# Kernel optimization log

Hardware: AMD Instinct MI355X
Metric: run time of the kernel (lower is better)

The kernel has to match this reference:

```python
import jax, jax.numpy as jnp
import numpy as np

B, T, N = 16, 1024, 512        # batch, time tokens, neurons
DK_T, DK_S = 64, 128           # key dims (temporal, spatial)
# dim_T = N, dim_S = T, dim_value_T = N (required by cross einsum), heads = 1


def setup_inputs() -> dict:
    key = jax.random.key(0)
    ks = jax.random.split(key, 11)
    return {
        "x_T": jax.random.normal(ks[0], (B, T, N), jnp.float32),
        "x_S": jax.random.normal(ks[1], (B, N, T), jnp.float32),
        "Wq_T": jax.random.normal(ks[2], (N, DK_T), jnp.float32) * 0.05,
        "Wk_T": jax.random.normal(ks[3], (N, DK_T), jnp.float32) * 0.05,
        "Wv_T": jax.random.normal(ks[4], (N, N), jnp.float32) * 0.05,
        "Wq_S": jax.random.normal(ks[5], (T, DK_S), jnp.float32) * 0.05,
        "Wk_S": jax.random.normal(ks[6], (T, DK_S), jnp.float32) * 0.05,
        "Wout_T": jax.random.normal(ks[7], (N, N), jnp.float32) * 0.05,
        "bout_T": jax.random.normal(ks[8], (N,), jnp.float32) * 0.05,
        "bias_T": jax.random.normal(ks[9], (1, 1, 1, DK_T), jnp.float32),
        "bias_S": jax.random.normal(ks[10], (1, 1, 1, DK_S), jnp.float32),
    }


def reference(x_T, x_S, Wq_T, Wk_T, Wv_T, Wq_S, Wk_S, Wout_T, bout_T, bias_T, bias_S):
    scale_T = DK_T ** -0.5
    scale_S = DK_S ** -0.5
    # Temporal attention: tokens along time axis, heads=1 -> add h axis
    q_T = (x_T @ Wq_T)[:, None] * scale_T          # [b,1,t,dk_T]
    k_T = (x_T @ Wk_T)[:, None]                    # [b,1,t,dk_T]
    v_T = (x_T @ Wv_T)[:, None]                    # [b,1,t,n]  (dim_value_T = n)
    logits_T = jnp.einsum('bhid,bhjd->bhij', q_T + bias_T, k_T)  # [b,1,t,t]
    attn_T = jax.nn.softmax(logits_T, axis=-1)
    out_T = jnp.einsum('bhij,bhjd->bhid', attn_T, v_T)            # [b,1,t,n]
    # Spatial attention: tokens along neuron axis
    q_S = (x_S @ Wq_S)[:, None] * scale_S          # [b,1,n,dk_S]
    k_S = (x_S @ Wk_S)[:, None]                    # [b,1,n,dk_S]
    logits_S = jnp.einsum('bhid,bhjd->bhij', q_S + bias_S, k_S)   # [b,1,n,n]
    attn_S = jax.nn.softmax(logits_S, axis=-1)
    # spatial_temporal_1 cross combination: attn_S mixes the neuron axis of out_T
    out_T = jnp.einsum('bhij,bhtj->bhti', attn_S, out_T)          # [b,1,t,n]
    out_T = out_T.reshape(B, T, N)                 # 'b h t d -> b t (h d)'
    out_T = out_T @ Wout_T + bout_T                # to_out_T
    return jnp.transpose(out_T, (0, 2, 1))         # [b, n, t]
```

## Files before the change

### kernel.cpp

```cpp
#include <hip/hip_runtime.h>
#include <cstddef>

typedef short short8 __attribute__((ext_vector_type(8)));
typedef unsigned short ushortx8 __attribute__((ext_vector_type(8)));
typedef unsigned short ushortx4 __attribute__((ext_vector_type(4)));
typedef float floatx4 __attribute__((ext_vector_type(4)));

__device__ __forceinline__ unsigned int bf16_rne(float x) {
    unsigned int u = __float_as_uint(x);
    return (u + 0x7fffu + ((u >> 16) & 1u)) >> 16;
}

__device__ __forceinline__ void split4(const floatx4 v,
                                       unsigned long long& hp,
                                       unsigned long long& lp) {
    unsigned int h[4], l[4];
    #pragma unroll
    for (int j = 0; j < 4; ++j) {
        h[j] = bf16_rne(v[j]);
        float hf = __uint_as_float(h[j] << 16);
        l[j] = bf16_rne(v[j] - hf);
    }
    hp = (unsigned long long)(h[0] | (h[1] << 16)) |
         ((unsigned long long)(h[2] | (h[3] << 16)) << 32);
    lp = (unsigned long long)(l[0] | (l[1] << 16)) |
         ((unsigned long long)(l[2] | (l[3] << 16)) << 32);
}

__device__ __forceinline__ unsigned long long pack_hi4(const floatx4 v) {
    unsigned int h0 = bf16_rne(v[0]), h1 = bf16_rne(v[1]);
    unsigned int h2 = bf16_rne(v[2]), h3 = bf16_rne(v[3]);
    return (unsigned long long)(h0 | (h1 << 16)) |
           ((unsigned long long)(h2 | (h3 << 16)) << 32);
}

__global__ __launch_bounds__(256)
void convert_split(const float* __restrict__ in, long n,
                   unsigned short* __restrict__ H, unsigned short* __restrict__ L)
{
    long n4 = n >> 2;
    for (long i = (long)blockIdx.x * 256 + threadIdx.x; i < n4;
         i += (long)gridDim.x * 256) {
        long e = i << 2;
        floatx4 v = *(const floatx4*)(in + e);
        ushortx4 h4, l4;
        #pragma unroll
        for (int j = 0; j < 4; ++j) {
            unsigned int h = bf16_rne(v[j]);
            float hf = __uint_as_float(h << 16);
            h4[j] = (unsigned short)h;
            l4[j] = (unsigned short)bf16_rne(v[j] - hf);
        }
        *(ushortx4*)(H + e) = h4;
        *(ushortx4*)(L + e) = l4;
    }
}

template<int BM, int BN, int AMODE, int BMODE, int OUTMODE, bool HASBIAS>
__global__ __launch_bounds__(256, 4)
void gemm_nt(const void* __restrict__ Ah_, const void* __restrict__ Al_,
             const void* __restrict__ Bh_, const void* __restrict__ Bl_,
             void* __restrict__ C_, void* __restrict__ Cl_,
             const float* __restrict__ bias,
             int K, int lda, int ldb, int ldc,
             long sA, long sB, long sC, float alpha, int nsplit, int mtiles)
{
    constexpr bool ALO = (AMODE == 1 || AMODE == 3);
    constexpr bool BLO = (BMODE == 1 || BMODE == 3);
    constexpr int LS = 40;
    __shared__ unsigned short Ash[2][BM][LS];
    __shared__ unsigned short Als[2][ALO ? BM : 1][LS];
    __shared__ unsigned short Bsh[2][BN][LS];
    __shared__ unsigned short Bls[2][BLO ? BN : 1][LS];

    const unsigned int gx = gridDim.x;
    const unsigned int nwg = gx * gridDim.y;
    unsigned int flat = blockIdx.y * gx + blockIdx.x;
    {
        unsigned int qq = nwg >> 3, rr = nwg & 7;
        unsigned int xcd = flat & 7, idx = flat >> 3;
        flat = (xcd < rr) ? (xcd * (qq + 1) + idx)
                          : (rr * (qq + 1) + (xcd - rr) * qq + idx);
    }
    const unsigned int perb = gx * (unsigned int)mtiles;
    const int b   = flat / perb;
    const unsigned int rm = flat % perb;
    const int bm0 = (rm / gx) * BM;
    const int bn0 = (rm % gx) * BN;
    const int tid  = threadIdx.x;
    const int lane = tid & 63;
    const int wid  = tid >> 6;
    const int wr = wid >> 1, wc = wid & 1;
    constexpr int WM = BM / 2, WN = BN / 2;
    constexpr int FM = WM / 16, FN = WN / 16;
    floatx4 acc[FM][FN] = {};
    const int l15  = lane & 15;
    const int koff = (lane >> 4) * 8;

    constexpr int ACHF = BM * 32 / 4, NAF0 = (ACHF + 255) / 256;
    constexpr int ACHH = BM * 32 / 8, NAH0 = (ACHH + 255) / 256;
    constexpr int BCHF = BN * 32 / 4, NBF0 = (BCHF + 255) / 256;
    constexpr int BCHH = BN * 32 / 8, NBH0 = (BCHH + 255) / 256;
    constexpr int NAF = (AMODE <= 1) ? NAF0 : 1;
    constexpr int NAH = (AMODE >= 2) ? NAH0 : 1;
    constexpr int NBF = (BMODE <= 1) ? NBF0 : 1;
    constexpr int NBH = (BMODE >= 2) ? NBH0 : 1;
    floatx4  aF[NAF], bF[NBF];
    ushortx8 aH[NAH], aL[NAH], bH[NBH], bL[NBH];

    auto loadA = [&](int k0) {
        if (AMODE <= 1) {
            const float* A = (const float*)Ah_ + (long)b * sA;
            #pragma unroll
            for (int i = 0; i < NAF; ++i) {
                int idx = i * 256 + tid;
                if (ACHF % 256 == 0 || idx < ACHF) {
                    int fc = idx * 4; int r = fc >> 5, c = fc & 31;
                    aF[i] = *(const floatx4*)(A + (long)(bm0 + r) * lda + k0 + c);
                }
            }
        } else {
            const unsigned short* A  = (const unsigned short*)Ah_ + (long)b * sA;
            const unsigned short* Al = (const unsigned short*)Al_ + (long)b * sA;
            #pragma unroll
            for (int i = 0; i < NAH; ++i) {
                int idx = i * 256 + tid;
                if (ACHH % 256 == 0 || idx < ACHH) {
                    int fc = idx * 8; int r = fc >> 5, c = fc & 31;
                    aH[i] = *(const ushortx8*)(A + (long)(bm0 + r) * lda + k0 + c);
                    if (AMODE == 3)
                        aL[i] = *(const ushortx8*)(Al + (long)(bm0 + r) * lda + k0 + c);
                }
            }
        }
    };
    auto loadB = [&](int k0) {
        if (BMODE <= 1) {
            const float* Bp = (const float*)Bh_ + (long)b * sB;
            #pragma unroll
            for (int i = 0; i < NBF; ++i) {
                int idx = i * 256 + tid;
                if (BCHF % 256 == 0 || idx < BCHF) {
                    int fc = idx * 4; int r = fc >> 5, c = fc & 31;
                    bF[i] = *(const floatx4*)(Bp + (long)(bn0 + r) * ldb + k0 + c);
                }
            }
        } else {
            const unsigned short* Bp = (const unsigned short*)Bh_ + (long)b * sB;
            const unsigned short* Bl = (const unsigned short*)Bl_ + (long)b * sB;
            #pragma unroll
            for (int i = 0; i < NBH; ++i) {
                int idx = i * 256 + tid;
                if (BCHH % 256 == 0 || idx < BCHH) {
                    int fc = idx * 8; int r = fc >> 5, c = fc & 31;
                    bH[i] = *(const ushortx8*)(Bp + (long)(bn0 + r) * ldb + k0 + c);
                    if (BMODE == 3)
                        bL[i] = *(const ushortx8*)(Bl + (long)(bn0 + r) * ldb + k0 + c);
                }
            }
        }
    };
    auto writeA = [&](int bf) {
        if (AMODE <= 1) {
            #pragma unroll
            for (int i = 0; i < NAF; ++i) {
                int idx = i * 256 + tid;
                if (ACHF % 256 == 0 || idx < ACHF) {
                    int fc = idx * 4; int r = fc >> 5, c = fc & 31;
                    if (AMODE == 1) {
                        unsigned long long hp, lp; split4(aF[i], hp, lp);
                        *(unsigned long long*)&Ash[bf][r][c] = hp;
                        *(unsigned long long*)&Als[bf][r][c] = lp;
                    } else {
                        *(unsigned long long*)&Ash[bf][r][c] = pack_hi4(aF[i]);
                    }
                }
            }
        } else {
            #pragma unroll
            for (int i = 0; i < NAH; ++i) {
                int idx = i * 256 + tid;
                if (ACHH % 256 == 0 || idx < ACHH) {
                    int fc = idx * 8; int r = fc >> 5, c = fc & 31;
                    *(ushortx8*)&Ash[bf][r][c] = aH[i];
                    if (AMODE == 3) *(ushortx8*)&Als[bf][r][c] = aL[i];
                }
            }
        }
    };
    auto writeB = [&](int bf) {
        if (BMODE <= 1) {
            #pragma unroll
            for (int i = 0; i < NBF; ++i) {
                int idx = i * 256 + tid;
                if (BCHF % 256 == 0 || idx < BCHF) {
                    int fc = idx * 4; int r = fc >> 5, c = fc & 31;
                    if (BMODE == 1) {
                        unsigned long long hp, lp; split4(bF[i], hp, lp);
                        *(unsigned long long*)&Bsh[bf][r][c] = hp;
                        *(unsigned long long*)&Bls[bf][r][c] = lp;
                    } else {
                        *(unsigned long long*)&Bsh[bf][r][c] = pack_hi4(bF[i]);
                    }
                }
            }
        } else {
            #pragma unroll
            for (int i = 0; i < NBH; ++i) {
                int idx = i * 256 + tid;
                if (BCHH % 256 == 0 || idx < BCHH) {
                    int fc = idx * 8; int r = fc >> 5, c = fc & 31;
                    *(ushortx8*)&Bsh[bf][r][c] = bH[i];
                    if (BMODE == 3) *(ushortx8*)&Bls[bf][r][c] = bL[i];
                }
            }
        }
    };
    auto compute = [&](int bf) {
        short8 ah[FM], al[FM], bh[FN], bl[FN];
        #pragma unroll
        for (int mi = 0; mi < FM; ++mi) {
            ah[mi] = *(const short8*)&Ash[bf][wr * WM + mi * 16 + l15][koff];
            if (ALO) al[mi] = *(const short8*)&Als[bf][wr * WM + mi * 16 + l15][koff];
        }
        #pragma unroll
        for (int ni = 0; ni < FN; ++ni) {
            bh[ni] = *(const short8*)&Bsh[bf][wc * WN + ni * 16 + l15][koff];
            if (BLO) bl[ni] = *(const short8*)&Bls[bf][wc * WN + ni * 16 + l15][koff];
        }
        #pragma unroll
        for (int mi = 0; mi < FM; ++mi)
            #pragma unroll
            for (int ni = 0; ni < FN; ++ni) {
                if (ALO)
                    acc[mi][ni] = __builtin_amdgcn_mfma_f32_16x16x32_bf16(
                        al[mi], bh[ni], acc[mi][ni], 0, 0, 0);
                if (BLO)
                    acc[mi][ni] = __builtin_amdgcn_mfma_f32_16x16x32_bf16(
                        ah[mi], bl[ni], acc[mi][ni], 0, 0, 0);
                acc[mi][ni] = __builtin_amdgcn_mfma_f32_16x16x32_bf16(
                    ah[mi], bh[ni], acc[mi][ni], 0, 0, 0);
            }
    };

    loadA(0); loadB(0);
    writeA(0); writeB(0);
    __syncthreads();
    int cur = 0;
    for (int k0 = 32; k0 < K; k0 += 32) {
        loadA(k0); loadB(k0);
        compute(cur);
        writeA(cur ^ 1); writeB(cur ^ 1);
        __syncthreads();
        cur ^= 1;
    }
    compute(cur);

    const int rq = (lane >> 4) * 4;
    #pragma unroll
    for (int mi = 0; mi < FM; ++mi) {
        #pragma unroll
        for (int ni = 0; ni < FN; ++ni) {
            int gm = bm0 + wr * WM + mi * 16 + rq;
            int gn = bn0 + wc * WN + ni * 16 + l15;
            float ae = (gn < nsplit) ? alpha : 1.0f;
            float be = 0.f;
            if (HASBIAS) be = (gn < nsplit) ? bias[gn] : 0.0f;
            float vals[4];
            #pragma unroll
            for (int j = 0; j < 4; ++j) vals[j] = acc[mi][ni][j] * ae + be;
            if (OUTMODE == 0) {
                float* C = (float*)C_ + (long)b * sC;
                #pragma unroll
                for (int j = 0; j < 4; ++j) C[(long)(gm + j) * ldc + gn] = vals[j];
            } else if (OUTMODE == 1) {
                float* C = (float*)C_ + (long)b * sC;
                floatx4 o;
                #pragma unroll
                for (int j = 0; j < 4; ++j) o[j] = vals[j];
                *(floatx4*)(C + (long)gn * ldc + gm) = o;
            } else if (OUTMODE == 2) {
                unsigned short* Ch = (unsigned short*)C_ + (long)b * sC;
                unsigned short* Cl = (unsigned short*)Cl_ + (long)b * sC;
                #pragma unroll
                for (int j = 0; j < 4; ++j) {
                    unsigned int h = bf16_rne(vals[j]);
                    float hf = __uint_as_float(h << 16);
                    unsigned int lo = bf16_rne(vals[j] - hf);
                    Ch[(long)(gm + j) * ldc + gn] = (unsigned short)h;
                    Cl[(long)(gm + j) * ldc + gn] = (unsigned short)lo;
                }
            } else {
                unsigned short* Ch = (unsigned short*)C_ + (long)b * sC;
                #pragma unroll
                for (int j = 0; j < 4; ++j)
                    Ch[(long)(gm + j) * ldc + gn] = (unsigned short)bf16_rne(vals[j]);
            }
        }
    }
}

template<int COLS, int DK, int LDQK, bool TRANSP>
__global__ __launch_bounds__(256, 2)
void qk_softmax(const unsigned short* __restrict__ qk_h,
                const unsigned short* __restrict__ qk_l,
                unsigned short* __restrict__ P)
{
    constexpr int WCOLS = COLS / 4;
    constexpr int FN = WCOLS / 16;
    constexpr int QPAD = DK + 24;
    __shared__ unsigned short Qh[32][QPAD];
    __shared__ unsigned short Ql[32][QPAD];
    __shared__ float red[32][4];
    __shared__ unsigned short Pl[32][COLS + 8];

    const int b  = blockIdx.y;
    const int q0 = blockIdx.x * 32;
    const long rowBase = (long)b * COLS;
    const int tid = threadIdx.x;
    const int lane = tid & 63, wid = tid >> 6;
    const int l15 = lane & 15, g = lane >> 4;
    const int koff = g * 8;

    constexpr int QCH = DK / 8;
    for (int i = tid; i < 32 * QCH; i += 256) {
        int r = i / QCH, c = (i % QCH) * 8;
        *(ushortx8*)&Qh[r][c] = *(const ushortx8*)(qk_h + (rowBase + q0 + r) * LDQK + c);
        *(ushortx8*)&Ql[r][c] = *(const ushortx8*)(qk_l + (rowBase + q0 + r) * LDQK + c);
    }
    __syncthreads();

    floatx4 acc[2][FN] = {};
    const unsigned short* kh = qk_h + rowBase * LDQK + DK;
    const unsigned short* kl = qk_l + rowBase * LDQK + DK;

    #pragma unroll
    for (int kk = 0; kk < DK; kk += 32) {
        short8 ah[2], al[2];
        #pragma unroll
        for (int mi = 0; mi < 2; ++mi) {
            ah[mi] = *(const short8*)&Qh[mi * 16 + l15][kk + koff];
            al[mi] = *(const short8*)&Ql[mi * 16 + l15][kk + koff];
        }
        #pragma unroll
        for (int ni = 0; ni < FN; ++ni) {
            long krow = wid * WCOLS + ni * 16 + l15;
            short8 bh = *(const short8*)(kh + krow * LDQK + kk + koff);
            short8 bl = *(const short8*)(kl + krow * LDQK + kk + koff);
            #pragma unroll
            for (int mi = 0; mi < 2; ++mi) {
                acc[mi][ni] = __builtin_amdgcn_mfma_f32_16x16x32_bf16(al[mi], bh, acc[mi][ni], 0, 0, 0);
                acc[mi][ni] = __builtin_amdgcn_mfma_f32_16x16x32_bf16(ah[mi], bl, acc[mi][ni], 0, 0, 0);
                acc[mi][ni] = __builtin_amdgcn_mfma_f32_16x16x32_bf16(ah[mi], bh, acc[mi][ni], 0, 0, 0);
            }
        }
    }

    float pm[2][4];
    #pragma unroll
    for (int mi = 0; mi < 2; ++mi)
        #pragma unroll
        for (int j = 0; j < 4; ++j) {
            float m = acc[mi][0][j];
            #pragma unroll
            for (int ni = 1; ni < FN; ++ni) m = fmaxf(m, acc[mi][ni][j]);
            pm[mi][j] = m;
        }
    #pragma unroll
    for (int msk = 1; msk < 16; msk <<= 1) {
        #pragma unroll
        for (int mi = 0; mi < 2; ++mi)
            #pragma unroll
            for (int j = 0; j < 4; ++j)
                pm[mi][j] = fmaxf(pm[mi][j], __shfl_xor(pm[mi][j], msk));
    }
    if (l15 == 0) {
        #pragma unroll
        for (int mi = 0; mi < 2; ++mi)
            #pragma unroll
            for (int j = 0; j < 4; ++j) red[mi * 16 + g * 4 + j][wid] = pm[mi][j];
    }
    __syncthreads();
    float rm[2][4];
    #pragma unroll
    for (int mi = 0; mi < 2; ++mi)
        #pragma unroll
        for (int j = 0; j < 4; ++j) {
            const float* r4 = red[mi * 16 + g * 4 + j];
            rm[mi][j] = fmaxf(fmaxf(r4[0], r4[1]), fmaxf(r4[2], r4[3]));
        }
    __syncthreads();

    float ps[2][4] = {};
    #pragma unroll
    for (int mi = 0; mi < 2; ++mi)
        #pragma unroll
        for (int ni = 0; ni < FN; ++ni)
            #pragma unroll
            for (int j = 0; j < 4; ++j) {
                float e = __expf(acc[mi][ni][j] - rm[mi][j]);
                acc[mi][ni][j] = e;
                ps[mi][j] += e;
            }
    #pragma unroll
    for (int msk = 1; msk < 16; msk <<= 1) {
        #pragma unroll
        for (int mi = 0; mi < 2; ++mi)
            #pragma unroll
            for (int j = 0; j < 4; ++j)
                ps[mi][j] += __shfl_xor(ps[mi][j], msk);
    }
    if (l15 == 0) {
        #pragma unroll
        for (int mi = 0; mi < 2; ++mi)
            #pragma unroll
            for (int j = 0; j < 4; ++j) red[mi * 16 + g * 4 + j][wid] = ps[mi][j];
    }
    __syncthreads();
    float inv[2][4];
    #pragma unroll
    for (int mi = 0; mi < 2; ++mi)
        #pragma unroll
        for (int j = 0; j < 4; ++j) {
            const float* r4 = red[mi * 16 + g * 4 + j];
            inv[mi][j] = 1.0f / (r4[0] + r4[1] + r4[2] + r4[3]);
        }

    #pragma unroll
    for (int mi = 0; mi < 2; ++mi)
        #pragma unroll
        for (int ni = 0; ni < FN; ++ni)
            #pragma unroll
            for (int j = 0; j < 4; ++j)
                Pl[mi * 16 + g * 4 + j][wid * WCOLS + ni * 16 + l15] =
                    (unsigned short)bf16_rne(acc[mi][ni][j] * inv[mi][j]);
    __syncthreads();

    if (TRANSP) {
        for (int i = tid; i < COLS * 4; i += 256) {
            int c = i >> 2;
            int rc = (i & 3) * 8;
            ushortx8 v;
            #pragma unroll
            for (int s = 0; s < 8; ++s) v[s] = Pl[rc + s][c];
            *(ushortx8*)(P + (rowBase + c) * COLS + q0 + rc) = v;
        }
    } else {
        constexpr int PCH = COLS / 8;
        for (int i = tid; i < 32 * PCH; i += 256) {
            int r = i / PCH, c = (i % PCH) * 8;
            *(ushortx8*)(P + (rowBase + q0 + r) * COLS + c) = *(const ushortx8*)&Pl[r][c];
        }
    }
}

__global__ __launch_bounds__(256)
void transpose_split(const float* __restrict__ in,
                     unsigned short* __restrict__ outH,
                     unsigned short* __restrict__ outL,
                     int R, int C, int rowOff, int ldo)
{
    __shared__ float tile[32][33];
    const int tc = blockIdx.x * 32, tr = blockIdx.y * 32;
    const int x = threadIdx.x, y = threadIdx.y;
    #pragma unroll
    for (int i = 0; i < 32; i += 8)
        tile[y + i][x] = in[(long)(tr + y + i) * C + tc + x];
    __syncthreads();
    #pragma unroll
    for (int i = 0; i < 32; i += 8) {
        float v = tile[x][y + i];
        unsigned int h = bf16_rne(v);
        float hf = __uint_as_float(h << 16);
        unsigned int lo = bf16_rne(v - hf);
        long idx = (long)(tc + y + i + rowOff) * ldo + tr + x;
        outH[idx] = (unsigned short)h;
        outL[idx] = (unsigned short)lo;
    }
}

extern "C" void kernel_launch(void* const* d_in, const int* in_sizes, int n_in,
                              void* d_out, int out_size, void* d_ws, size_t ws_size,
                              hipStream_t stream)
{
    (void)in_sizes; (void)n_in; (void)out_size; (void)ws_size;
    const float* x_T    = (const float*)d_in[0];
    const float* x_S    = (const float*)d_in[1];
    const float* Wq_T   = (const float*)d_in[2];
    const float* Wk_T   = (const float*)d_in[3];
    const float* Wv_T   = (const float*)d_in[4];
    const float* Wq_S   = (const float*)d_in[5];
    const float* Wk_S   = (const float*)d_in[6];
    const float* Wout_T = (const float*)d_in[7];
    const float* bout_T = (const float*)d_in[8];
    const float* bias_T = (const float*)d_in[9];
    const float* bias_S = (const float*)d_in[10];
    float* out = (float*)d_out;

    constexpr int B = 16, T = 1024, N = 512, DKT = 64, DKS = 128;
    typedef unsigned short us;

    char* w = (char*)d_ws;
    size_t off = 0;
    auto alloc = [&](size_t bytes) { char* p = w + off; off = (off + bytes + 255) & ~(size_t)255; return p; };
    us* wqkT_h = (us*)alloc(128 * 512 * 2);
    us* wqkT_l = (us*)alloc(128 * 512 * 2);
    us* wvt_h  = (us*)alloc(512 * 512 * 2);
    us* wvt_l  = (us*)alloc(512 * 512 * 2);
    us* wqks_h = (us*)alloc(256 * 1024 * 2);
    us* wqks_l = (us*)alloc(256 * 1024 * 2);
    us* wout_h = (us*)alloc(512 * 512 * 2);
    us* wout_l = (us*)alloc(512 * 512 * 2);
    us* qk_h   = (us*)alloc((size_t)16384 * 128 * 2);
    us* qk_l   = (us*)alloc((size_t)16384 * 128 * 2);
    us* P_T    = (us*)alloc((size_t)B * T * T * 2);
    us* P_St   = (us*)alloc((size_t)B * N * N * 2);
    us* vT_h   = (us*)alloc((size_t)B * N * T * 2);
    us* vT_l   = (us*)alloc((size_t)B * N * T * 2);
    us* outT_h = (us*)alloc((size_t)B * T * N * 2);
    us* outT_l = (us*)alloc((size_t)B * T * N * 2);
    us* x_h    = (us*)alloc((size_t)16384 * 512 * 2);
    us* x_l    = (us*)alloc((size_t)16384 * 512 * 2);
    us* M1t_h  = vT_l;

    const float scale_T = 0.125f;
    const float scale_S = 0.088388347648318447f;
    const int BIG = 1 << 30;
    const long XE = (long)16384 * 512;

    dim3 tb(32, 8);
    transpose_split<<<dim3(2, 16),  tb, 0, stream>>>(Wq_T,   wqkT_h, wqkT_l, 512, 64,   0, 512);
    transpose_split<<<dim3(2, 16),  tb, 0, stream>>>(Wk_T,   wqkT_h, wqkT_l, 512, 64,  64, 512);
    transpose_split<<<dim3(16, 16), tb, 0, stream>>>(Wv_T,   wvt_h,  wvt_l,  512, 512,  0, 512);
    transpose_split<<<dim3(4, 32),  tb, 0, stream>>>(Wq_S,   wqks_h, wqks_l, 1024, 128, 0, 1024);
    transpose_split<<<dim3(4, 32),  tb, 0, stream>>>(Wk_S,   wqks_h, wqks_l, 1024, 128, 128, 1024);
    transpose_split<<<dim3(16, 16), tb, 0, stream>>>(Wout_T, wout_h, wout_l, 512, 512,  0, 512);

    convert_split<<<2048, 256, 0, stream>>>(x_T, XE, x_h, x_l);
    gemm_nt<64, 64, 3, 3, 2, true><<<dim3(2, 256), 256, 0, stream>>>(
        x_h, x_l, wqkT_h, wqkT_l, qk_h, qk_l, bias_T,
        512, 512, 512, 128, 0, 0, 0, scale_T, 64, 256);
    gemm_nt<64, 128, 3, 2, 3, false><<<dim3(8, 8 * B), 256, 0, stream>>>(
        wvt_h, wvt_l, x_h, nullptr, vT_h, nullptr, nullptr,
        512, 512, 512, 1024, 0, (long)T * N, (long)N * T, 1.0f, 0, 8);
    qk_softmax<1024, 64, 128, false><<<dim3(32, 16), 256, 0, stream>>>(qk_h, qk_l, P_T);
    gemm_nt<64, 128, 2, 2, 2, false><<<dim3(4, 16 * B), 256, 0, stream>>>(
        P_T, nullptr, vT_h, nullptr, outT_h, outT_l, nullptr,
        1024, 1024, 1024, 512, (long)T * T, (long)N * T, (long)T * N, 1.0f, 0, 16);

    convert_split<<<2048, 256, 0, stream>>>(x_S, XE, x_h, x_l);
    gemm_nt<64, 64, 3, 3, 2, true><<<dim3(4, 128), 256, 0, stream>>>(
        x_h, x_l, wqks_h, wqks_l, qk_h, qk_l, bias_S,
        1024, 1024, 1024, 256, 0, 0, 0, scale_S, 128, 128);
    qk_softmax<512, 128, 256, true><<<dim3(16, 16), 256, 0, stream>>>(qk_h, qk_l, P_St);
    gemm_nt<64, 128, 3, 2, 3, false><<<dim3(4, 8 * B), 256, 0, stream>>>(
        wout_h, wout_l, P_St, nullptr, M1t_h, nullptr, nullptr,
        512, 512, 512, 512, 0, (long)N * N, (long)N * N, 1.0f, 0, 8);
    gemm_nt<64, 128, 3, 2, 1, true><<<dim3(4, 16 * B), 256, 0, stream>>>(
        outT_h, outT_l, M1t_h, nullptr, out, nullptr, bout_T,
        512, 512, 512, 1024, (long)T * N, (long)N * N, (long)N * T, 1.0f, BIG, 16);
}
```

Measured before the change: 223.9 us.

## Fuse temporal softmax with PV matmul and batch weight/input conversions

The temporal QK softmax kernel now performs the P·V matmul itself, reading V directly from global memory, so the B×T×T probability matrix is never written to or re-read from global memory. The six weight transposes are merged into one launch, and both input conversions into another. The final GEMM drops the low-part split of outT, which reduces precision there. The fused PV loop has no shared-memory staging of V and runs only 512 blocks, so it may be limited by memory latency or occupancy.

```diff
diff --git a/kernel.cpp b/kernel.cpp
--- a/kernel.cpp
+++ b/kernel.cpp
@@ -34,15 +34,66 @@
            ((unsigned long long)(h2 | (h3 << 16)) << 32);
 }
 
+__device__ __forceinline__ unsigned int xcd_swz(unsigned int flat, unsigned int nwg) {
+    unsigned int qq = nwg >> 3, rr = nwg & 7;
+    unsigned int xcd = flat & 7, idx = flat >> 3;
+    return (xcd < rr) ? (xcd * (qq + 1) + idx)
+                      : (rr * (qq + 1) + (xcd - rr) * qq + idx);
+}
+
 __global__ __launch_bounds__(256)
-void convert_split(const float* __restrict__ in, long n,
-                   unsigned short* __restrict__ H, unsigned short* __restrict__ L)
+void transpose_split_all(const float* __restrict__ WqT, const float* __restrict__ WkT,
+                         const float* __restrict__ Wv,  const float* __restrict__ WqS,
+                         const float* __restrict__ WkS, const float* __restrict__ Wout,
+                         unsigned short* __restrict__ wqkT_h, unsigned short* __restrict__ wqkT_l,
+                         unsigned short* __restrict__ wvt_h,  unsigned short* __restrict__ wvt_l,
+                         unsigned short* __restrict__ wqks_h, unsigned short* __restrict__ wqks_l,
+                         unsigned short* __restrict__ wout_h, unsigned short* __restrict__ wout_l)
+{
+    int bid = blockIdx.x;
+    const float* in; unsigned short *oh, *ol;
+    int R, C, rowOff, ldo, gxx;
+    if (bid < 32)       { in = WqT;  oh = wqkT_h; ol = wqkT_l; R = 512;  C = 64;  rowOff = 0;   ldo = 512;  gxx = 2;  }
+    else if (bid < 64)  { in = WkT;  oh = wqkT_h; ol = wqkT_l; R = 512;  C = 64;  rowOff = 64;  ldo = 512;  gxx = 2;  bid -= 32;  }
+    else if (bid < 320) { in = Wv;   oh = wvt_h;  ol = wvt_l;  R = 512;  C = 512; rowOff = 0;   ldo = 512;  gxx = 16; bid -= 64;  }
+    else if (bid < 448) { in = WqS;  oh = wqks_h; ol = wqks_l; R = 1024; C = 128; rowOff = 0;   ldo = 1024; gxx = 4;  bid -= 320; }
+    else if (bid < 576) { in = WkS;  oh = wqks_h; ol = wqks_l; R = 1024; C = 128; rowOff = 128; ldo = 1024; gxx = 4;  bid -= 448; }
+    else                { in = Wout; oh = wout_h; ol = wout_l; R = 512;  C = 512; rowOff = 0;   ldo = 512;  gxx = 16; bid -= 576; }
+
+    __shared__ float tile[32][33];
+    const int tc = (bid % gxx) * 32, tr = (bid / gxx) * 32;
+    const int x = threadIdx.x, y = threadIdx.y;
+    #pragma unroll
+    for (int i = 0; i < 32; i += 8)
+        tile[y + i][x] = in[(long)(tr + y + i) * C + tc + x];
+    __syncthreads();
+    #pragma unroll
+    for (int i = 0; i < 32; i += 8) {
+        float v = tile[x][y + i];
+        unsigned int h = bf16_rne(v);
+        float hf = __uint_as_float(h << 16);
+        unsigned int lo = bf16_rne(v - hf);
+        long idx = (long)(tc + y + i + rowOff) * ldo + tr + x;
+        oh[idx] = (unsigned short)h;
+        ol[idx] = (unsigned short)lo;
+    }
+}
+
+__global__ __launch_bounds__(256)
+void convert_both(const float* __restrict__ a, const float* __restrict__ bsrc, long n,
+                  unsigned short* __restrict__ Ha, unsigned short* __restrict__ La,
+                  unsigned short* __restrict__ Hb, unsigned short* __restrict__ Lb)
 {
     long n4 = n >> 2;
-    for (long i = (long)blockIdx.x * 256 + threadIdx.x; i < n4;
+    long tot = n4 * 2;
+    for (long i = (long)blockIdx.x * 256 + threadIdx.x; i < tot;
          i += (long)gridDim.x * 256) {
-        long e = i << 2;
-        floatx4 v = *(const floatx4*)(in + e);
+        bool second = i >= n4;
+        long e = (second ? i - n4 : i) << 2;
+        const float* src = second ? bsrc : a;
+        unsigned short* H = second ? Hb : Ha;
+        unsigned short* L = second ? Lb : La;
+        floatx4 v = *(const floatx4*)(src + e);
         ushortx4 h4, l4;
         #pragma unroll
         for (int j = 0; j < 4; ++j) {
@@ -74,14 +125,7 @@
     __shared__ unsigned short Bls[2][BLO ? BN : 1][LS];
 
     const unsigned int gx = gridDim.x;
-    const unsigned int nwg = gx * gridDim.y;
-    unsigned int flat = blockIdx.y * gx + blockIdx.x;
-    {
-        unsigned int qq = nwg >> 3, rr = nwg & 7;
-        unsigned int xcd = flat & 7, idx = flat >> 3;
-        flat = (xcd < rr) ? (xcd * (qq + 1) + idx)
-                          : (rr * (qq + 1) + (xcd - rr) * qq + idx);
-    }
+    unsigned int flat = xcd_swz(blockIdx.y * gx + blockIdx.x, gx * gridDim.y);
     const unsigned int perb = gx * (unsigned int)mtiles;
     const int b   = flat / perb;
     const unsigned int rm = flat % perb;
@@ -300,11 +344,180 @@
     }
 }
 
-template<int COLS, int DK, int LDQK, bool TRANSP>
 __global__ __launch_bounds__(256, 2)
-void qk_softmax(const unsigned short* __restrict__ qk_h,
-                const unsigned short* __restrict__ qk_l,
-                unsigned short* __restrict__ P)
+void qk_sm_pv(const unsigned short* __restrict__ qk_h,
+              const unsigned short* __restrict__ qk_l,
+              const unsigned short* __restrict__ vT,
+              unsigned short* __restrict__ outT)
+{
+    constexpr int COLS = 1024, DK = 64, LDQK = 128, NOUT = 512;
+    constexpr int WCOLS = COLS / 4;
+    constexpr int FN = WCOLS / 16;
+    constexpr int QPAD = DK + 24;
+    __shared__ unsigned short Qh[32][QPAD];
+    __shared__ unsigned short Ql[32][QPAD];
+    __shared__ float red[32][4];
+    __shared__ unsigned short Pl[32][COLS + 8];
+
+    const unsigned int gx = gridDim.x;
+    unsigned int flat = xcd_swz(blockIdx.y * gx + blockIdx.x, gx * gridDim.y);
+    const int b  = flat / gx;
+    const int q0 = (flat % gx) * 32;
+    const long rowBase = (long)b * COLS;
+    const int tid = threadIdx.x;
+    const int lane = tid & 63, wid = tid >> 6;
+    const int l15 = lane & 15, g = lane >> 4;
+    const int koff = g * 8;
+
+    constexpr int QCH = DK / 8;
+    for (int i = tid; i < 32 * QCH; i += 256) {
+        int r = i / QCH, c = (i % QCH) * 8;
+        *(ushortx8*)&Qh[r][c] = *(const ushortx8*)(qk_h + (rowBase + q0 + r) * LDQK + c);
+        *(ushortx8*)&Ql[r][c] = *(const ushortx8*)(qk_l + (rowBase + q0 + r) * LDQK + c);
+    }
+    __syncthreads();
+
+    {
+        floatx4 acc[2][FN] = {};
+        const unsigned short* kh = qk_h + rowBase * LDQK + DK;
+        const unsigned short* kl = qk_l + rowBase * LDQK + DK;
+
+        #pragma unroll
+        for (int kk = 0; kk < DK; kk += 32) {
+            short8 ah[2], al[2];
+            #pragma unroll
+            for (int mi = 0; mi < 2; ++mi) {
+                ah[mi] = *(const short8*)&Qh[mi * 16 + l15][kk + koff];
+                al[mi] = *(const short8*)&Ql[mi * 16 + l15][kk + koff];
+            }
+            #pragma unroll
+            for (int ni = 0; ni < FN; ++ni) {
+                long krow = wid * WCOLS + ni * 16 + l15;
+                short8 bh = *(const short8*)(kh + krow * LDQK + kk + koff);
+                short8 bl = *(const short8*)(kl + krow * LDQK + kk + koff);
+                #pragma unroll
+                for (int mi = 0; mi < 2; ++mi) {
+                    acc[mi][ni] = __builtin_amdgcn_mfma_f32_16x16x32_bf16(al[mi], bh, acc[mi][ni], 0, 0, 0);
+                    acc[mi][ni] = __builtin_amdgcn_mfma_f32_16x16x32_bf16(ah[mi], bl, acc[mi][ni], 0, 0, 0);
+                    acc[mi][ni] = __builtin_amdgcn_mfma_f32_16x16x32_bf16(ah[mi], bh, acc[mi][ni], 0, 0, 0);
+                }
+            }
+        }
+
+        float pm[2][4];
+        #pragma unroll
+        for (int mi = 0; mi < 2; ++mi)
+            #pragma unroll
+            for (int j = 0; j < 4; ++j) {
+                float m = acc[mi][0][j];
+                #pragma unroll
+                for (int ni = 1; ni < FN; ++ni) m = fmaxf(m, acc[mi][ni][j]);
+                pm[mi][j] = m;
+            }
+        #pragma unroll
+        for (int msk = 1; msk < 16; msk <<= 1) {
+            #pragma unroll
+            for (int mi = 0; mi < 2; ++mi)
+                #pragma unroll
+                for (int j = 0; j < 4; ++j)
+                    pm[mi][j] = fmaxf(pm[mi][j], __shfl_xor(pm[mi][j], msk));
+        }
+        if (l15 == 0) {
+            #pragma unroll
+            for (int mi = 0; mi < 2; ++mi)
+                #pragma unroll
+                for (int j = 0; j < 4; ++j) red[mi * 16 + g * 4 + j][wid] = pm[mi][j];
+        }
+        __syncthreads();
+        float rm[2][4];
+        #pragma unroll
+        for (int mi = 0; mi < 2; ++mi)
+            #pragma unroll
+            for (int j = 0; j < 4; ++j) {
+                const float* r4 = red[mi * 16 + g * 4 + j];
+                rm[mi][j] = fmaxf(fmaxf(r4[0], r4[1]), fmaxf(r4[2], r4[3]));
+            }
+        __syncthreads();
+
+        float ps[2][4] = {};
+        #pragma unroll
+        for (int mi = 0; mi < 2; ++mi)
+            #pragma unroll
+            for (int ni = 0; ni < FN; ++ni)
+                #pragma unroll
+                for (int j = 0; j < 4; ++j) {
+                    float e = __expf(acc[mi][ni][j] - rm[mi][j]);
+                    acc[mi][ni][j] = e;
+                    ps[mi][j] += e;
+                }
+        #pragma unroll
+        for (int msk = 1; msk < 16; msk <<= 1) {
+            #pragma unroll
+            for (int mi = 0; mi < 2; ++mi)
+                #pragma unroll
+                for (int j = 0; j < 4; ++j)
+                    ps[mi][j] += __shfl_xor(ps[mi][j], msk);
+        }
+        if (l15 == 0) {
+            #pragma unroll
+            for (int mi = 0; mi < 2; ++mi)
+                #pragma unroll
+                for (int j = 0; j < 4; ++j) red[mi * 16 + g * 4 + j][wid] = ps[mi][j];
+        }
+        __syncthreads();
+        float inv[2][4];
+        #pragma unroll
+        for (int mi = 0; mi < 2; ++mi)
+            #pragma unroll
+            for (int j = 0; j < 4; ++j) {
+                const float* r4 = red[mi * 16 + g * 4 + j];
+                inv[mi][j] = 1.0f / (r4[0] + r4[1] + r4[2] + r4[3]);
+            }
+
+        #pragma unroll
+        for (int mi = 0; mi < 2; ++mi)
+            #pragma unroll
+            for (int ni = 0; ni < FN; ++ni)
+                #pragma unroll
+                for (int j = 0; j < 4; ++j)
+                    Pl[mi * 16 + g * 4 + j][wid * WCOLS + ni * 16 + l15] =
+                        (unsigned short)bf16_rne(acc[mi][ni][j] * inv[mi][j]);
+    }
+    __syncthreads();
+
+    const unsigned short* vh = vT + (long)b * NOUT * COLS;
+    floatx4 acc2[2][8] = {};
+    for (int kk = 0; kk < COLS; kk += 32) {
+        short8 pa[2];
+        pa[0] = *(const short8*)&Pl[l15][kk + koff];
+        pa[1] = *(const short8*)&Pl[16 + l15][kk + koff];
+        #pragma unroll
+        for (int ni = 0; ni < 8; ++ni) {
+            long n = wid * 128 + ni * 16 + l15;
+            short8 bh = *(const short8*)(vh + n * COLS + kk + koff);
+            acc2[0][ni] = __builtin_amdgcn_mfma_f32_16x16x32_bf16(pa[0], bh, acc2[0][ni], 0, 0, 0);
+            acc2[1][ni] = __builtin_amdgcn_mfma_f32_16x16x32_bf16(pa[1], bh, acc2[1][ni], 0, 0, 0);
+        }
+    }
+    unsigned short* op = outT + (long)b * COLS * NOUT;
+    #pragma unroll
+    for (int mi = 0; mi < 2; ++mi)
+        #pragma unroll
+        for (int ni = 0; ni < 8; ++ni) {
+            int gn = wid * 128 + ni * 16 + l15;
+            #pragma unroll
+            for (int j = 0; j < 4; ++j) {
+                int gt = q0 + mi * 16 + g * 4 + j;
+                op[(long)gt * NOUT + gn] = (unsigned short)bf16_rne(acc2[mi][ni][j]);
+            }
+        }
+}
+
+template<int COLS, int DK, int LDQK>
+__global__ __launch_bounds__(256, 2)
+void qk_softmax_t(const unsigned short* __restrict__ qk_h,
+                  const unsigned short* __restrict__ qk_l,
+                  unsigned short* __restrict__ P)
 {
     constexpr int WCOLS = COLS / 4;
     constexpr int FN = WCOLS / 16;
@@ -314,8 +527,10 @@
     __shared__ float red[32][4];
     __shared__ unsigned short Pl[32][COLS + 8];
 
-    const int b  = blockIdx.y;
-    const int q0 = blockIdx.x * 32;
+    const unsigned int gx = gridDim.x;
+    unsigned int flat = xcd_swz(blockIdx.y * gx + blockIdx.x, gx * gridDim.y);
+    const int b  = flat / gx;
+    const int q0 = (flat % gx) * 32;
     const long rowBase = (long)b * COLS;
     const int tid = threadIdx.x;
     const int lane = tid & 63, wid = tid >> 6;
@@ -436,46 +651,13 @@
                     (unsigned short)bf16_rne(acc[mi][ni][j] * inv[mi][j]);
     __syncthreads();
 
-    if (TRANSP) {
-        for (int i = tid; i < COLS * 4; i += 256) {
-            int c = i >> 2;
-            int rc = (i & 3) * 8;
-            ushortx8 v;
-            #pragma unroll
-            for (int s = 0; s < 8; ++s) v[s] = Pl[rc + s][c];
-            *(ushortx8*)(P + (rowBase + c) * COLS + q0 + rc) = v;
-        }
-    } else {
-        constexpr int PCH = COLS / 8;
-        for (int i = tid; i < 32 * PCH; i += 256) {
-            int r = i / PCH, c = (i % PCH) * 8;
-            *(ushortx8*)(P + (rowBase + q0 + r) * COLS + c) = *(const ushortx8*)&Pl[r][c];
-        }
-    }
-}
-
-__global__ __launch_bounds__(256)
-void transpose_split(const float* __restrict__ in,
-                     unsigned short* __restrict__ outH,
-                     unsigned short* __restrict__ outL,
-                     int R, int C, int rowOff, int ldo)
-{
-    __shared__ float tile[32][33];
-    const int tc = blockIdx.x * 32, tr = blockIdx.y * 32;
-    const int x = threadIdx.x, y = threadIdx.y;
-    #pragma unroll
-    for (int i = 0; i < 32; i += 8)
-        tile[y + i][x] = in[(long)(tr + y + i) * C + tc + x];
-    __syncthreads();
-    #pragma unroll
-    for (int i = 0; i < 32; i += 8) {
-        float v = tile[x][y + i];
-        unsigned int h = bf16_rne(v);
-        float hf = __uint_as_float(h << 16);
-        unsigned int lo = bf16_rne(v - hf);
-        long idx = (long)(tc + y + i + rowOff) * ldo + tr + x;
-        outH[idx] = (unsigned short)h;
-        outL[idx] = (unsigned short)lo;
+    for (int i = tid; i < COLS * 4; i += 256) {
+        int c = i >> 2;
+        int rc = (i & 3) * 8;
+        ushortx8 v;
+        #pragma unroll
+        for (int s = 0; s < 8; ++s) v[s] = Pl[rc + s][c];
+        *(ushortx8*)(P + (rowBase + c) * COLS + q0 + rc) = v;
     }
 }
 
@@ -513,50 +695,41 @@
     us* wout_l = (us*)alloc(512 * 512 * 2);
     us* qk_h   = (us*)alloc((size_t)16384 * 128 * 2);
     us* qk_l   = (us*)alloc((size_t)16384 * 128 * 2);
-    us* P_T    = (us*)alloc((size_t)B * T * T * 2);
     us* P_St   = (us*)alloc((size_t)B * N * N * 2);
     us* vT_h   = (us*)alloc((size_t)B * N * T * 2);
-    us* vT_l   = (us*)alloc((size_t)B * N * T * 2);
+    us* M1t_h  = (us*)alloc((size_t)B * N * N * 2);
     us* outT_h = (us*)alloc((size_t)B * T * N * 2);
-    us* outT_l = (us*)alloc((size_t)B * T * N * 2);
-    us* x_h    = (us*)alloc((size_t)16384 * 512 * 2);
-    us* x_l    = (us*)alloc((size_t)16384 * 512 * 2);
-    us* M1t_h  = vT_l;
+    us* xT_h   = (us*)alloc((size_t)16384 * 512 * 2);
+    us* xT_l   = (us*)alloc((size_t)16384 * 512 * 2);
+    us* xS_h   = (us*)alloc((size_t)16384 * 512 * 2);
+    us* xS_l   = (us*)alloc((size_t)16384 * 512 * 2);
 
     const float scale_T = 0.125f;
     const float scale_S = 0.088388347648318447f;
     const int BIG = 1 << 30;
     const long XE = (long)16384 * 512;
 
-    dim3 tb(32, 8);
-    transpose_split<<<dim3(2, 16),  tb, 0, stream>>>(Wq_T,   wqkT_h, wqkT_l, 512, 64,   0, 512);
-    transpose_split<<<dim3(2, 16),  tb, 0, stream>>>(Wk_T,   wqkT_h, wqkT_l, 512, 64,  64, 512);
-    transpose_split<<<dim3(16, 16), tb, 0, stream>>>(Wv_T,   wvt_h,  wvt_l,  512, 512,  0, 512);
-    transpose_split<<<dim3(4, 32),  tb, 0, stream>>>(Wq_S,   wqks_h, wqks_l, 1024, 128, 0, 1024);
-    transpose_split<<<dim3(4, 32),  tb, 0, stream>>>(Wk_S,   wqks_h, wqks_l, 1024, 128, 128, 1024);
-    transpose_split<<<dim3(16, 16), tb, 0, stream>>>(Wout_T, wout_h, wout_l, 512, 512,  0, 512);
-
-    convert_split<<<2048, 256, 0, stream>>>(x_T, XE, x_h, x_l);
+    transpose_split_all<<<832, dim3(32, 8), 0, stream>>>(
+        Wq_T, Wk_T, Wv_T, Wq_S, Wk_S, Wout_T,
+        wqkT_h, wqkT_l, wvt_h, wvt_l, wqks_h, wqks_l, wout_h, wout_l);
+    convert_both<<<4096, 256, 0, stream>>>(x_T, x_S, XE, xT_h, xT_l, xS_h, xS_l);
+
     gemm_nt<64, 64, 3, 3, 2, true><<<dim3(2, 256), 256, 0, stream>>>(
-        x_h, x_l, wqkT_h, wqkT_l, qk_h, qk_l, bias_T,
+        xT_h, xT_l, wqkT_h, wqkT_l, qk_h, qk_l, bias_T,
         512, 512, 512, 128, 0, 0, 0, scale_T, 64, 256);
     gemm_nt<64, 128, 3, 2, 3, false><<<dim3(8, 8 * B), 256, 0, stream>>>(
-        wvt_h, wvt_l, x_h, nullptr, vT_h, nullptr, nullptr,
+        wvt_h, wvt_l, xT_h, nullptr, vT_h, nullptr, nullptr,
         512, 512, 512, 1024, 0, (long)T * N, (long)N * T, 1.0f, 0, 8);
-    qk_softmax<1024, 64, 128, false><<<dim3(32, 16), 256, 0, stream>>>(qk_h, qk_l, P_T);
-    gemm_nt<64, 128, 2, 2, 2, false><<<dim3(4, 16 * B), 256, 0, stream>>>(
-        P_T, nullptr, vT_h, nullptr, outT_h, outT_l, nullptr,
-        1024, 1024, 1024, 512, (long)T * T, (long)N * T, (long)T * N, 1.0f, 0, 16);
-
-    convert_split<<<2048, 256, 0, stream>>>(x_S, XE, x_h, x_l);
+    qk_sm_pv<<<dim3(32, 16), 256, 0, stream>>>(qk_h, qk_l, vT_h, outT_h);
+
     gemm_nt<64, 64, 3, 3, 2, true><<<dim3(4, 128), 256, 0, stream>>>(
-        x_h, x_l, wqks_h, wqks_l, qk_h, qk_l, bias_S,
+        xS_h, xS_l, wqks_h, wqks_l, qk_h, qk_l, bias_S,
         1024, 1024, 1024, 256, 0, 0, 0, scale_S, 128, 128);
-    qk_softmax<512, 128, 256, true><<<dim3(16, 16), 256, 0, stream>>>(qk_h, qk_l, P_St);
+    qk_softmax_t<512, 128, 256><<<dim3(16, 16), 256, 0, stream>>>(qk_h, qk_l, P_St);
     gemm_nt<64, 128, 3, 2, 3, false><<<dim3(4, 8 * B), 256, 0, stream>>>(
         wout_h, wout_l, P_St, nullptr, M1t_h, nullptr, nullptr,
         512, 512, 512, 512, 0, (long)N * N, (long)N * N, 1.0f, 0, 8);
-    gemm_nt<64, 128, 3, 2, 1, true><<<dim3(4, 16 * B), 256, 0, stream>>>(
-        outT_h, outT_l, M1t_h, nullptr, out, nullptr, bout_T,
+    gemm_nt<64, 128, 2, 2, 1, true><<<dim3(4, 16 * B), 256, 0, stream>>>(
+        outT_h, nullptr, M1t_h, nullptr, out, nullptr, bout_T,
         512, 512, 512, 1024, (long)T * N, (long)N * N, (long)N * T, 1.0f, BIG, 16);
 }
```

After: 224.0 us. About the same (+0.0%).
